# Optimization experiments

Hardware: AMD Instinct MI355X
Metric: run time of the kernel (lower is better)

## Reference

```python
import jax, jax.numpy as jnp
import numpy as np

N = 8192       # number of graph nodes (A.shape[0])
D_IN = 256     # input_dim
D_THETA = 256  # hard-coded theta projection dim
D_OUT = 256    # output_dim
K = 5          # per-row top-k sparsification
BN_EPS = 1e-5
LRELU_SLOPE = 0.01


def setup_inputs() -> dict:
    key = jax.random.key(0)
    k0, k1, k2 = jax.random.split(key, 3)
    H = jax.random.normal(k0, (N, D_IN), dtype=jnp.float32)
    # Linear(input_dim, 256)
    W_theta = jax.random.normal(k1, (D_IN, D_THETA), dtype=jnp.float32) * (1.0 / np.sqrt(D_IN))
    b_theta = jnp.zeros((D_THETA,), dtype=jnp.float32)
    # Linear(input_dim, output_dim)
    W_out = jax.random.normal(k2, (D_IN, D_OUT), dtype=jnp.float32) * (1.0 / np.sqrt(D_IN))
    b_out = jnp.zeros((D_OUT,), dtype=jnp.float32)
    # BatchNorm1d(input_dim) affine params (fresh init)
    bn_gamma = jnp.ones((D_IN,), dtype=jnp.float32)
    bn_beta = jnp.zeros((D_IN,), dtype=jnp.float32)
    return {"H": H, "bn_gamma": bn_gamma, "bn_beta": bn_beta,
            "W_theta": W_theta, "b_theta": b_theta,
            "W_out": W_out, "b_out": b_out}


def reference(H, bn_gamma, bn_beta, W_theta, b_theta, W_out, b_out):
    # BatchNorm1d in training mode: biased batch stats over the node axis
    mu = H.mean(axis=0)
    var = H.var(axis=0)  # biased, matching torch normalization
    Hn = (H - mu) * jax.lax.rsqrt(var + BN_EPS) * bn_gamma + bn_beta  # [N, D_IN]

    # theta projection -> SAM affinity
    Hx = Hn @ W_theta + b_theta                                        # [N, D_THETA]
    nrm = jnp.maximum(jnp.linalg.norm(Hx, axis=1, keepdims=True), 1e-12)  # F.normalize eps
    F1 = Hx / nrm
    dist = jnp.clip(F1 @ F1.T, -1.0, 1.0)                              # [N, N]
    sam = jnp.nan_to_num(jnp.arccos(dist))
    # original SAM() detaches (numpy round-trip): affinity is a constant wrt grads
    sam = jax.lax.stop_gradient(sam)

    A = jnp.maximum(jax.nn.sigmoid(jnp.exp(-0.2 * sam)), 0.1)          # clamp(min=0.1)

    # per-row top-k sparsification (fused replacement of the python double loop)
    _, idx = jax.lax.top_k(A, K)                                       # [N, K]
    mask = jnp.zeros_like(A).at[jnp.arange(N)[:, None], idx].set(1.0)
    A = A * mask

    # D^{-1/2} A D^{-1/2} without materializing diag matrices
    dinv = A.sum(axis=1) ** -0.5                                       # [N]
    A_hat = dinv[:, None] * A * dinv[None, :]

    out = A_hat @ (Hn @ W_out + b_out)                                 # [N, D_OUT]
    out = jnp.where(out >= 0, out, LRELU_SLOPE * out)                  # LeakyReLU
    return out, A
```

## Files before the change

### kernel.cpp

```cpp
#include <hip/hip_runtime.h>
#include <hip/hip_bf16.h>
#include <cstdint>
#include <cstddef>

#define NN 8192
#define DD 256

using bf16 = __hip_bfloat16;
typedef unsigned short ushort_t;
typedef unsigned int uint32;
typedef short short8 __attribute__((ext_vector_type(8)));
typedef float f32x4 __attribute__((ext_vector_type(4)));

#define GL2LDS(g, l) __builtin_amdgcn_global_load_lds( \
  (const __attribute__((address_space(1))) void*)(g),  \
  (__attribute__((address_space(3))) void*)(l), 16, 0, 0)

__device__ __forceinline__ float ldin(const void* p, int flag, size_t i) {
  return flag ? __bfloat162float(((const bf16*)p)[i]) : ((const float*)p)[i];
}

__device__ __forceinline__ void ins8(float v, int jj, float (&lv)[8], int (&li)[8]) {
  if (v <= lv[7]) return;
  int cnt = 0;
#pragma unroll
  for (int s = 0; s < 8; ++s) cnt += (lv[s] >= v) ? 1 : 0;
#pragma unroll
  for (int s = 7; s >= 1; --s) {
    bool sh = (s > cnt);
    lv[s] = sh ? lv[s-1] : lv[s];
    li[s] = sh ? li[s-1] : li[s];
  }
#pragma unroll
  for (int s = 0; s < 8; ++s) if (s == cnt) { lv[s] = v; li[s] = jj; }
}

__device__ __forceinline__ void ins8t(float v, int jj, float (&lv)[8], int (&li)[8]) {
  bool lose = (lv[7] > v) || (lv[7] == v && li[7] < jj);
  if (lose) return;
  int cnt = 0;
#pragma unroll
  for (int s = 0; s < 8; ++s) cnt += ((lv[s] > v) || (lv[s] == v && li[s] < jj)) ? 1 : 0;
#pragma unroll
  for (int s = 7; s >= 1; --s) {
    bool sh = (s > cnt);
    lv[s] = sh ? lv[s-1] : lv[s];
    li[s] = sh ? li[s-1] : li[s];
  }
#pragma unroll
  for (int s = 0; s < 8; ++s) if (s == cnt) { lv[s] = v; li[s] = jj; }
}

__device__ __forceinline__ bool lexgt(float va, int ia, float vb, int ib) {
  return (va > vb) || (va == vb && ia < ib);
}

__global__ void k_detect(const ushort_t* __restrict__ Hu, int* __restrict__ flag) {
  __shared__ int cnt;
  if (threadIdx.x == 0) cnt = 0;
  __syncthreads();
  int sane = 0;
  for (int u = 0; u < 16; ++u) {
    int idx = 2 * (threadIdx.x * 16 + u);
    ushort_t h = Hu[idx];
    int e = (h >> 7) & 0xFF;
    sane += (e >= 113 && e <= 133) ? 1 : 0;
  }
  atomicAdd(&cnt, sane);
  __syncthreads();
  if (threadIdx.x == 0) *flag = (cnt > 2048) ? 1 : 0;
}

__global__ void k_transposeH(const void* __restrict__ H, const int* __restrict__ pflag,
                             float* __restrict__ HT) {
  int flag = *pflag;
  __shared__ float tile[64][65];
  int i0 = blockIdx.x * 64;
  int c0 = blockIdx.y * 64;
  int tid = threadIdx.x;
  int r = tid >> 2, cb = (tid & 3) * 16;
#pragma unroll
  for (int u = 0; u < 16; ++u)
    tile[r][cb + u] = ldin(H, flag, (size_t)(i0 + r) * DD + c0 + cb + u);
  __syncthreads();
  int c = tid >> 2, rb = (tid & 3) * 16;
#pragma unroll
  for (int u4 = 0; u4 < 4; ++u4) {
    float4 t;
    t.x = tile[rb + 4*u4 + 0][c];
    t.y = tile[rb + 4*u4 + 1][c];
    t.z = tile[rb + 4*u4 + 2][c];
    t.w = tile[rb + 4*u4 + 3][c];
    *(float4*)&HT[(size_t)(c0 + c) * NN + i0 + rb + 4*u4] = t;
  }
}

__global__ __launch_bounds__(256) void k_statsT(const float* __restrict__ HT,
                                                float* __restrict__ mu32, float* __restrict__ rs32) {
  __shared__ float buf[8192];
  int c = blockIdx.x;
  int tid = threadIdx.x;
#pragma unroll
  for (int it = 0; it < 8; ++it) {
    int idx = it * 1024 + tid * 4;
    *(float4*)&buf[idx] = *(const float4*)&HT[(size_t)c * NN + idx];
  }
  __syncthreads();
  if (tid == 0) {
    float acc = 0.0f;
    for (int r = 0; r < 8192; r += 32) {
      float4 v[8];
#pragma unroll
      for (int q = 0; q < 8; ++q) v[q] = *(const float4*)&buf[r + q * 4];
#pragma unroll
      for (int q = 0; q < 8; ++q) {
        acc = __fadd_rn(acc, v[q].x);
        acc = __fadd_rn(acc, v[q].y);
        acc = __fadd_rn(acc, v[q].z);
        acc = __fadd_rn(acc, v[q].w);
      }
    }
    float mu = __fdiv_rn(acc, 8192.0f);
    float vacc = 0.0f;
    for (int r = 0; r < 8192; r += 32) {
      float4 v[8];
#pragma unroll
      for (int q = 0; q < 8; ++q) v[q] = *(const float4*)&buf[r + q * 4];
#pragma unroll
      for (int q = 0; q < 8; ++q) {
        float d0 = __fsub_rn(v[q].x, mu); vacc = __fadd_rn(vacc, __fmul_rn(d0, d0));
        float d1 = __fsub_rn(v[q].y, mu); vacc = __fadd_rn(vacc, __fmul_rn(d1, d1));
        float d2 = __fsub_rn(v[q].z, mu); vacc = __fadd_rn(vacc, __fmul_rn(d2, d2));
        float d3 = __fsub_rn(v[q].w, mu); vacc = __fadd_rn(vacc, __fmul_rn(d3, d3));
      }
    }
    float var = __fdiv_rn(vacc, 8192.0f);
    mu32[c] = mu;
    rs32[c] = __fdiv_rn(1.0f, sqrtf(__fadd_rn(var, 1e-5f)));
  }
}

__global__ void k_bn32(const void* __restrict__ H, const int* __restrict__ pflag,
                       const float* __restrict__ mu32, const float* __restrict__ rs32,
                       const void* __restrict__ gamma, const void* __restrict__ beta,
                       float* __restrict__ Hn) {
  int flag = *pflag;
  int i = blockIdx.x, c = threadIdx.x;
  float t = __fsub_rn(ldin(H, flag, (size_t)i * DD + c), mu32[c]);
  t = __fmul_rn(t, rs32[c]);
  t = __fmul_rn(t, ldin(gamma, flag, c));
  t = __fadd_rn(t, ldin(beta, flag, c));
  Hn[(size_t)i * DD + c] = t;
}

__global__ __launch_bounds__(256) void k_hx(const float* __restrict__ Hn,
    const void* __restrict__ Wt, const void* __restrict__ bt, const int* __restrict__ pflag,
    float* __restrict__ Hx) {
  int flag = *pflag;
  __shared__ float sHn[DD];
  int i = blockIdx.x, n = threadIdx.x;
  sHn[n] = Hn[(size_t)i * DD + n];
  __syncthreads();
  float acc = 0.0f;
#pragma unroll 8
  for (int k = 0; k < DD; ++k)
    acc = fmaf(sHn[k], ldin(Wt, flag, (size_t)k * DD + n), acc);
  Hx[(size_t)i * DD + n] = __fadd_rn(acc, ldin(bt, flag, n));
}

__global__ void k_norm32(float* __restrict__ F1, ushort_t* __restrict__ F1hi,
                         ushort_t* __restrict__ F1lo) {
  int w = threadIdx.x >> 6, lane = threadIdx.x & 63;
  int row = blockIdx.x * 4 + w;
  float* x = F1 + (size_t)row * DD;
  float part = 0.0f;
  if (lane < 16) {
    int base = (lane >> 3) * 128 + (lane & 7);
    float e0 = x[base];
    part = __fmul_rn(e0, e0);
#pragma unroll
    for (int t = 1; t < 16; ++t) {
      float e = x[base + 8 * t];
      part = __fadd_rn(part, __fmul_rn(e, e));
    }
  }
  float p[16];
#pragma unroll
  for (int s = 0; s < 16; ++s) p[s] = __shfl(part, s, 64);
  float P1 = __fadd_rn(__fadd_rn(__fadd_rn(p[0], p[1]), __fadd_rn(p[2], p[3])),
                       __fadd_rn(__fadd_rn(p[4], p[5]), __fadd_rn(p[6], p[7])));
  float P2 = __fadd_rn(__fadd_rn(__fadd_rn(p[8], p[9]), __fadd_rn(p[10], p[11])),
                       __fadd_rn(__fadd_rn(p[12], p[13]), __fadd_rn(p[14], p[15])));
  float nrm = fmaxf(sqrtf(__fadd_rn(P1, P2)), 1e-12f);
#pragma unroll
  for (int u = 0; u < 4; ++u) {
    float xn = __fdiv_rn(x[lane * 4 + u], nrm);
    x[lane * 4 + u] = xn;
    bf16 hi = __float2bfloat16(xn);
    float lo = __fsub_rn(xn, __bfloat162float(hi));
    F1hi[(size_t)row * DD + lane * 4 + u] = *(ushort_t*)&hi;
    bf16 lob = __float2bfloat16(lo);
    F1lo[(size_t)row * DD + lane * 4 + u] = *(ushort_t*)&lob;
  }
}

__global__ __launch_bounds__(256) void k_gemm_s(
    const ushort_t* __restrict__ F1hi, const ushort_t* __restrict__ F1lo,
    int jc, float* __restrict__ S) {
  __shared__ __align__(16) ushort_t AH[4096];
  __shared__ __align__(16) ushort_t AL[4096];
  __shared__ __align__(16) ushort_t BH[4096];
  __shared__ __align__(16) ushort_t BL[4096];
  const int tid = threadIdx.x;
  const int w = tid >> 6, lane = tid & 63;
  const int quad = lane >> 4, l15 = lane & 15;
  const int wi = w >> 1, wj = w & 1;
  const int i0 = blockIdx.y * 128;
  const int j0loc = blockIdx.x * 128;
  const int j0 = jc * 2048 + j0loc;

  const int rofs = lane >> 2;
  const int ccl  = (lane & 3) ^ (rofs & 3);
  const int laneElem = rofs * DD + ccl * 8;

  f32x4 acc[4][4];
#pragma unroll
  for (int fr = 0; fr < 4; ++fr)
#pragma unroll
    for (int fc = 0; fc < 4; ++fc) acc[fr][fc] = (f32x4)0.0f;

  for (int chunk = 0; chunk < 8; ++chunk) {
    const int kofs = chunk * 32;
    __syncthreads();
#pragma unroll
    for (int q = 0; q < 2; ++q) {
      const int s = w * 2 + q;
      const size_t ga = (size_t)(i0 + s * 16) * DD + kofs;
      const size_t gb = (size_t)(j0 + s * 16) * DD + kofs;
      GL2LDS(F1hi + ga + laneElem, &AH[s * 512]);
      GL2LDS(F1lo + ga + laneElem, &AL[s * 512]);
      GL2LDS(F1hi + gb + laneElem, &BH[s * 512]);
      GL2LDS(F1lo + gb + laneElem, &BL[s * 512]);
    }
    __syncthreads();
    short8 ah[4], al[4], bh[4], bl[4];
#pragma unroll
    for (int fr = 0; fr < 4; ++fr) {
      int row = wi * 64 + fr * 16 + l15;
      int g = quad ^ (row & 3);
      ah[fr] = *(const short8*)&AH[row * 32 + g * 8];
      al[fr] = *(const short8*)&AL[row * 32 + g * 8];
    }
#pragma unroll
    for (int fc = 0; fc < 4; ++fc) {
      int row = wj * 64 + fc * 16 + l15;
      int g = quad ^ (row & 3);
      bh[fc] = *(const short8*)&BH[row * 32 + g * 8];
      bl[fc] = *(const short8*)&BL[row * 32 + g * 8];
    }
#pragma unroll
    for (int fr = 0; fr < 4; ++fr)
#pragma unroll
      for (int fc = 0; fc < 4; ++fc) {
        acc[fr][fc] = __builtin_amdgcn_mfma_f32_16x16x32_bf16(ah[fr], bh[fc], acc[fr][fc], 0, 0, 0);
        acc[fr][fc] = __builtin_amdgcn_mfma_f32_16x16x32_bf16(ah[fr], bl[fc], acc[fr][fc], 0, 0, 0);
        acc[fr][fc] = __builtin_amdgcn_mfma_f32_16x16x32_bf16(al[fr], bh[fc], acc[fr][fc], 0, 0, 0);
      }
  }
#pragma unroll
  for (int fr = 0; fr < 4; ++fr) {
#pragma unroll
    for (int reg = 0; reg < 4; ++reg) {
      int row = i0 + wi * 64 + fr * 16 + quad * 4 + reg;
#pragma unroll
      for (int fc = 0; fc < 4; ++fc) {
        int coll = j0loc + wj * 64 + fc * 16 + l15;
        S[(size_t)row * 2048 + coll] = acc[fr][fc][reg];
      }
    }
  }
}

__global__ __launch_bounds__(256) void k_scan(const float* __restrict__ S, int jc,
                                              float* __restrict__ candv, int* __restrict__ candi) {
  int w = threadIdx.x >> 6, lane = threadIdx.x & 63;
  int row = blockIdx.x * 4 + w;
  const int jbase = jc * 2048;
  float lv[8]; int li[8];
#pragma unroll
  for (int e = 0; e < 8; ++e) { lv[e] = -3.0e38f; li[e] = 0x7fffffff; }
  const float* p = S + (size_t)row * 2048;
#pragma unroll
  for (int it = 0; it < 8; ++it) {
    int col = it * 256 + lane * 4;
    float4 v = *(const float4*)&p[col];
    ins8(v.x, jbase + col + 0, lv, li);
    ins8(v.y, jbase + col + 1, lv, li);
    ins8(v.z, jbase + col + 2, lv, li);
    ins8(v.w, jbase + col + 3, lv, li);
  }
#pragma unroll
  for (int m = 1; m <= 32; m <<= 1) {
    float bv[8]; int bi[8];
#pragma unroll
    for (int e = 0; e < 8; ++e) {
      bv[e] = __shfl_xor(lv[e], m, 64);
      bi[e] = __shfl_xor(li[e], m, 64);
    }
#pragma unroll
    for (int e = 0; e < 8; ++e) {
      bool t = lexgt(lv[e], li[e], bv[7 - e], bi[7 - e]);
      lv[e] = t ? lv[e] : bv[7 - e];
      li[e] = t ? li[e] : bi[7 - e];
    }
#pragma unroll
    for (int d = 4; d >= 1; d >>= 1) {
#pragma unroll
      for (int e = 0; e < 8; ++e) {
        if ((e & d) == 0) {
          int f = e + d;
          bool sw = lexgt(lv[f], li[f], lv[e], li[e]);
          float tv = lv[e]; int ti = li[e];
          lv[e] = sw ? lv[f] : lv[e];  li[e] = sw ? li[f] : li[e];
          lv[f] = sw ? tv : lv[f];     li[f] = sw ? ti : li[f];
        }
      }
    }
  }
  if (lane == 0) {
    size_t base = ((size_t)row * 4 + jc) * 8;
#pragma unroll
    for (int e = 0; e < 8; ++e) { candv[base + e] = lv[e]; candi[base + e] = li[e]; }
  }
}

__global__ void k_merge(const float* __restrict__ candv, const int* __restrict__ candi,
                        int* __restrict__ cand8) {
  int row = blockIdx.x * 256 + threadIdx.x;
  float bv[8]; int bj[8];
#pragma unroll
  for (int e = 0; e < 8; ++e) { bv[e] = -3.0e38f; bj[e] = 0x7fffffff; }
  for (int t = 0; t < 32; ++t) {
    float v = candv[(size_t)row * 32 + t];
    int j   = candi[(size_t)row * 32 + t];
    ins8t(v, j, bv, bj);
  }
#pragma unroll
  for (int e = 0; e < 8; ++e) cand8[row * 8 + e] = bj[e];
}

__global__ void k_rerank(const float* __restrict__ F1, const int* __restrict__ cand8,
                         int* __restrict__ top5i, float* __restrict__ top5v,
                         float* __restrict__ dinv) {
  int w = threadIdx.x >> 6, lane = threadIdx.x & 63;
  int row = blockIdx.x * 4 + w;
  int jl = 0x7fffffff;
  float a32 = -1.0f;
  if (lane < 8) {
    jl = cand8[row * 8 + lane];
    const float* xi = F1 + (size_t)row * DD;
    const float* xj = F1 + (size_t)jl * DD;
    float acc = 0.0f;
#pragma unroll 8
    for (int k = 0; k < DD; ++k)
      acc = fmaf(xi[k], xj[k], acc);
    float d = fminf(fmaxf(acc, -1.0f), 1.0f);
    float sam = acosf(d);
    float xx = expf(__fmul_rn(-0.2f, sam));
    float sig = __fdiv_rn(1.0f, __fadd_rn(1.0f, expf(-xx)));
    a32 = fmaxf(sig, 0.1f);
  }
  float av[8]; int aj[8];
#pragma unroll
  for (int l = 0; l < 8; ++l) { av[l] = __shfl(a32, l, 64); aj[l] = __shfl(jl, l, 64); }
  if (lane == 0) {
    bool used[8] = {false,false,false,false,false,false,false,false};
    double dsum = 0.0;
#pragma unroll
    for (int k = 0; k < 5; ++k) {
      float bv = -2.0f; int bj = 0x7fffffff; int bs = -1;
#pragma unroll
      for (int s = 0; s < 8; ++s) {
        bool better = (!used[s]) && ((av[s] > bv) || (av[s] == bv && aj[s] < bj));
        bs = better ? s : bs;
        bv = better ? av[s] : bv;
        bj = better ? aj[s] : bj;
      }
#pragma unroll
      for (int s = 0; s < 8; ++s) used[s] = used[s] || (s == bs);
      top5i[row * 5 + k] = bj;
      top5v[row * 5 + k] = bv;
      dsum += (double)bv;
    }
    dinv[row] = (float)(1.0 / sqrt(dsum));
  }
}

__global__ void k_z(const float* __restrict__ Hn, const int* __restrict__ top5i,
                    const float* __restrict__ top5v, const float* __restrict__ dinv,
                    float* __restrict__ Z, float* __restrict__ srow) {
  __shared__ int sj[5];
  __shared__ float sw[5];
  int i = blockIdx.x, tid = threadIdx.x;
  if (tid < 5) {
    int j = top5i[i * 5 + tid];
    sj[tid] = j;
    sw[tid] = dinv[i] * top5v[i * 5 + tid] * dinv[j];
  }
  __syncthreads();
  double z = 0.0;
#pragma unroll
  for (int k = 0; k < 5; ++k) z += (double)sw[k] * (double)Hn[(size_t)sj[k] * DD + tid];
  Z[(size_t)i * DD + tid] = (float)z;
  if (tid == 0) srow[i] = sw[0] + sw[1] + sw[2] + sw[3] + sw[4];
}

__global__ __launch_bounds__(256) void k_out3(const float* __restrict__ Z,
    const void* __restrict__ Wo, const void* __restrict__ bo,
    const float* __restrict__ srow, const int* __restrict__ pflag, void* __restrict__ outp) {
  int flag = *pflag;
  __shared__ float sZ[DD];
  int i = blockIdx.x, n = threadIdx.x;
  sZ[n] = Z[(size_t)i * DD + n];
  __syncthreads();
  float acc = 0.0f;
#pragma unroll 8
  for (int k = 0; k < DD; ++k)
    acc = fmaf(sZ[k], ldin(Wo, flag, (size_t)k * DD + n), acc);
  float v = acc + srow[i] * ldin(bo, flag, n);
  v = (v >= 0.0f) ? v : 0.01f * v;
  if (flag) ((bf16*)outp)[(size_t)i * DD + n] = __float2bfloat16(v);
  else      ((float*)outp)[(size_t)i * DD + n] = v;
}

__global__ void k_zeroA(void* __restrict__ d_out, const int* __restrict__ pflag) {
  int flag = *pflag;
  size_t esize = flag ? 2 : 4;
  uint4* base = (uint4*)((char*)d_out + (size_t)NN * DD * esize);
  size_t n16 = ((size_t)NN * NN * esize) >> 4;
  size_t idx = (size_t)blockIdx.x * 256 + threadIdx.x;
  size_t stride = (size_t)gridDim.x * 256;
  uint4 z; z.x = 0; z.y = 0; z.z = 0; z.w = 0;
  for (size_t i = idx; i < n16; i += stride) base[i] = z;
}

__global__ void k_scatter(void* __restrict__ d_out, const int* __restrict__ pflag,
                          const int* __restrict__ top5i, const float* __restrict__ top5v) {
  int flag = *pflag;
  int t = blockIdx.x * 256 + threadIdx.x;
  if (t >= NN * 5) return;
  int row = t / 5, k = t % 5;
  int col = top5i[row * 5 + k];
  float v = top5v[row * 5 + k];
  size_t off = (size_t)row * NN + col;
  if (flag) ((bf16*)((char*)d_out + (size_t)NN * DD * 2))[off] = __float2bfloat16(v);
  else      ((float*)((char*)d_out + (size_t)NN * DD * 4))[off] = v;
}

extern "C" void kernel_launch(void* const* d_in, const int* in_sizes, int n_in,
                              void* d_out, int out_size, void* d_ws, size_t ws_size,
                              hipStream_t stream) {
  (void)in_sizes; (void)n_in; (void)out_size; (void)ws_size;
  const void* H     = d_in[0];
  const void* gamma = d_in[1];
  const void* beta  = d_in[2];
  const void* Wt    = d_in[3];
  const void* bt    = d_in[4];
  const void* Wo    = d_in[5];
  const void* bo    = d_in[6];

  const size_t MB = 1048576;
  char* zb = (char*)d_out + 8 * MB;
  float*    Hn32  = (float*)(zb + 0);
  float*    F1_32 = (float*)(zb + 8 * MB);
  ushort_t* F1hi  = (ushort_t*)(zb + 16 * MB);
  ushort_t* F1lo  = (ushort_t*)(zb + 20 * MB);
  float*    candv = (float*)(zb + 24 * MB);
  int*      candi = (int*)(zb + 25 * MB);
  float*    Z32   = (float*)(zb + 28 * MB);
  float*    HT    = (float*)(zb + 36 * MB);
  float*    mu32  = (float*)(zb + 44 * MB);
  float*    rs32  = (float*)(zb + 44 * MB + 4096);
  int*      cand8 = (int*)(zb + 44 * MB + 8192);
  float*    dinv  = (float*)(zb + 44 * MB + 270336);
  float*    srow  = (float*)(zb + 44 * MB + 303104);
  float*    Schunk= (float*)(zb + 48 * MB);

  char* ws = (char*)d_ws;
  int*   flag  = (int*)(ws + 0);
  int*   top5i = (int*)(ws + 256);
  float* top5v = (float*)(ws + 164096);

  k_detect<<<dim3(1), dim3(256), 0, stream>>>((const ushort_t*)H, flag);
  k_transposeH<<<dim3(128, 4), dim3(256), 0, stream>>>(H, flag, HT);
  k_statsT<<<dim3(256), dim3(256), 0, stream>>>(HT, mu32, rs32);
  k_bn32<<<dim3(NN), dim3(256), 0, stream>>>(H, flag, mu32, rs32, gamma, beta, Hn32);
  k_hx<<<dim3(NN), dim3(256), 0, stream>>>(Hn32, Wt, bt, flag, F1_32);
  k_norm32<<<dim3(2048), dim3(256), 0, stream>>>(F1_32, F1hi, F1lo);
  for (int jc = 0; jc < 4; ++jc) {
    k_gemm_s<<<dim3(16, 64), dim3(256), 0, stream>>>(F1hi, F1lo, jc, Schunk);
    k_scan<<<dim3(2048), dim3(256), 0, stream>>>(Schunk, jc, candv, candi);
  }
  k_merge<<<dim3(32), dim3(256), 0, stream>>>(candv, candi, cand8);
  k_rerank<<<dim3(2048), dim3(256), 0, stream>>>(F1_32, cand8, top5i, top5v, dinv);
  k_z<<<dim3(NN), dim3(256), 0, stream>>>(Hn32, top5i, top5v, dinv, Z32, srow);
  k_out3<<<dim3(NN), dim3(256), 0, stream>>>(Z32, Wo, bo, srow, flag, d_out);
  k_zeroA<<<dim3(8192), dim3(256), 0, stream>>>(d_out, flag);
  k_scatter<<<dim3(160), dim3(256), 0, stream>>>(d_out, flag, top5i, top5v);
}
```

Baseline: 930.8 us.

## Fuse BN/projection/normalize, Z/output, zero/scatter kernels; skip scan inserts early

Merges the batchnorm, theta projection and row-normalization into one kernel that handles 8 rows per block, so each weight load is reused across 8 rows and the intermediate Hx no longer goes through global memory. It likewise fuses the neighbor aggregation with the output projection, 8 rows per block, and combines zeroing of the dense A matrix with the top-5 scatter, one pass per row pair. The scan adds a max-of-4 test so whole float4 groups that cannot enter the top-8 skip insertion. Risks are lower occupancy from the larger shared arrays and register accumulators, plus a different write pattern for the large A zero-fill.

```diff
diff --git a/kernel.cpp b/kernel.cpp
--- a/kernel.cpp
+++ b/kernel.cpp
@@ -140,67 +140,77 @@
   }
 }
 
-__global__ void k_bn32(const void* __restrict__ H, const int* __restrict__ pflag,
-                       const float* __restrict__ mu32, const float* __restrict__ rs32,
-                       const void* __restrict__ gamma, const void* __restrict__ beta,
-                       float* __restrict__ Hn) {
+__global__ __launch_bounds__(256) void k_hxn(const void* __restrict__ H,
+    const int* __restrict__ pflag, const float* __restrict__ mu32, const float* __restrict__ rs32,
+    const void* __restrict__ gamma, const void* __restrict__ beta,
+    const void* __restrict__ Wt, const void* __restrict__ bt,
+    float* __restrict__ Hn, float* __restrict__ F1,
+    ushort_t* __restrict__ F1hi, ushort_t* __restrict__ F1lo) {
   int flag = *pflag;
-  int i = blockIdx.x, c = threadIdx.x;
-  float t = __fsub_rn(ldin(H, flag, (size_t)i * DD + c), mu32[c]);
-  t = __fmul_rn(t, rs32[c]);
-  t = __fmul_rn(t, ldin(gamma, flag, c));
-  t = __fadd_rn(t, ldin(beta, flag, c));
-  Hn[(size_t)i * DD + c] = t;
-}
-
-__global__ __launch_bounds__(256) void k_hx(const float* __restrict__ Hn,
-    const void* __restrict__ Wt, const void* __restrict__ bt, const int* __restrict__ pflag,
-    float* __restrict__ Hx) {
-  int flag = *pflag;
-  __shared__ float sHn[DD];
-  int i = blockIdx.x, n = threadIdx.x;
-  sHn[n] = Hn[(size_t)i * DD + n];
-  __syncthreads();
-  float acc = 0.0f;
+  __shared__ float sHn[8][256];
+  __shared__ float sHx[8][256];
+  __shared__ float sp[8][16];
+  __shared__ float snrm[8];
+  const int r0 = blockIdx.x * 8;
+  const int n = threadIdx.x;
+  float g  = ldin(gamma, flag, n);
+  float b  = ldin(beta, flag, n);
+  float mu = mu32[n], rs = rs32[n];
+#pragma unroll
+  for (int r = 0; r < 8; ++r) {
+    float t = __fsub_rn(ldin(H, flag, (size_t)(r0 + r) * DD + n), mu);
+    t = __fmul_rn(t, rs);
+    t = __fmul_rn(t, g);
+    t = __fadd_rn(t, b);
+    sHn[r][n] = t;
+    Hn[(size_t)(r0 + r) * DD + n] = t;
+  }
+  __syncthreads();
+  float acc[8];
+#pragma unroll
+  for (int r = 0; r < 8; ++r) acc[r] = 0.0f;
 #pragma unroll 8
-  for (int k = 0; k < DD; ++k)
-    acc = fmaf(sHn[k], ldin(Wt, flag, (size_t)k * DD + n), acc);
-  Hx[(size_t)i * DD + n] = __fadd_rn(acc, ldin(bt, flag, n));
-}
-
-__global__ void k_norm32(float* __restrict__ F1, ushort_t* __restrict__ F1hi,
-                         ushort_t* __restrict__ F1lo) {
-  int w = threadIdx.x >> 6, lane = threadIdx.x & 63;
-  int row = blockIdx.x * 4 + w;
-  float* x = F1 + (size_t)row * DD;
-  float part = 0.0f;
-  if (lane < 16) {
-    int base = (lane >> 3) * 128 + (lane & 7);
-    float e0 = x[base];
-    part = __fmul_rn(e0, e0);
+  for (int k = 0; k < DD; ++k) {
+    float w = ldin(Wt, flag, (size_t)k * DD + n);
+#pragma unroll
+    for (int r = 0; r < 8; ++r) acc[r] = fmaf(sHn[r][k], w, acc[r]);
+  }
+  float btn = ldin(bt, flag, n);
+#pragma unroll
+  for (int r = 0; r < 8; ++r) sHx[r][n] = __fadd_rn(acc[r], btn);
+  __syncthreads();
+  if (n < 128) {
+    int r = n >> 4, s = n & 15;
+    int base = (s >> 3) * 128 + (s & 7);
+    float e0 = sHx[r][base];
+    float part = __fmul_rn(e0, e0);
 #pragma unroll
     for (int t = 1; t < 16; ++t) {
-      float e = x[base + 8 * t];
+      float e = sHx[r][base + 8 * t];
       part = __fadd_rn(part, __fmul_rn(e, e));
     }
-  }
-  float p[16];
-#pragma unroll
-  for (int s = 0; s < 16; ++s) p[s] = __shfl(part, s, 64);
-  float P1 = __fadd_rn(__fadd_rn(__fadd_rn(p[0], p[1]), __fadd_rn(p[2], p[3])),
-                       __fadd_rn(__fadd_rn(p[4], p[5]), __fadd_rn(p[6], p[7])));
-  float P2 = __fadd_rn(__fadd_rn(__fadd_rn(p[8], p[9]), __fadd_rn(p[10], p[11])),
-                       __fadd_rn(__fadd_rn(p[12], p[13]), __fadd_rn(p[14], p[15])));
-  float nrm = fmaxf(sqrtf(__fadd_rn(P1, P2)), 1e-12f);
-#pragma unroll
-  for (int u = 0; u < 4; ++u) {
-    float xn = __fdiv_rn(x[lane * 4 + u], nrm);
-    x[lane * 4 + u] = xn;
+    sp[r][s] = part;
+  }
+  __syncthreads();
+  if (n < 8) {
+    const float* p = sp[n];
+    float P1 = __fadd_rn(__fadd_rn(__fadd_rn(p[0], p[1]), __fadd_rn(p[2], p[3])),
+                         __fadd_rn(__fadd_rn(p[4], p[5]), __fadd_rn(p[6], p[7])));
+    float P2 = __fadd_rn(__fadd_rn(__fadd_rn(p[8], p[9]), __fadd_rn(p[10], p[11])),
+                         __fadd_rn(__fadd_rn(p[12], p[13]), __fadd_rn(p[14], p[15])));
+    snrm[n] = fmaxf(sqrtf(__fadd_rn(P1, P2)), 1e-12f);
+  }
+  __syncthreads();
+#pragma unroll
+  for (int r = 0; r < 8; ++r) {
+    float xn = __fdiv_rn(sHx[r][n], snrm[r]);
+    size_t idx = (size_t)(r0 + r) * DD + n;
+    F1[idx] = xn;
     bf16 hi = __float2bfloat16(xn);
     float lo = __fsub_rn(xn, __bfloat162float(hi));
-    F1hi[(size_t)row * DD + lane * 4 + u] = *(ushort_t*)&hi;
+    F1hi[idx] = *(ushort_t*)&hi;
     bf16 lob = __float2bfloat16(lo);
-    F1lo[(size_t)row * DD + lane * 4 + u] = *(ushort_t*)&lob;
+    F1lo[idx] = *(ushort_t*)&lob;
   }
 }
 
@@ -294,10 +304,13 @@
   for (int it = 0; it < 8; ++it) {
     int col = it * 256 + lane * 4;
     float4 v = *(const float4*)&p[col];
-    ins8(v.x, jbase + col + 0, lv, li);
-    ins8(v.y, jbase + col + 1, lv, li);
-    ins8(v.z, jbase + col + 2, lv, li);
-    ins8(v.w, jbase + col + 3, lv, li);
+    float m4 = fmaxf(fmaxf(v.x, v.y), fmaxf(v.z, v.w));
+    if (m4 > lv[7]) {
+      ins8(v.x, jbase + col + 0, lv, li);
+      ins8(v.y, jbase + col + 1, lv, li);
+      ins8(v.z, jbase + col + 2, lv, li);
+      ins8(v.w, jbase + col + 3, lv, li);
+    }
   }
 #pragma unroll
   for (int m = 1; m <= 32; m <<= 1) {
@@ -396,65 +409,72 @@
   }
 }
 
-__global__ void k_z(const float* __restrict__ Hn, const int* __restrict__ top5i,
-                    const float* __restrict__ top5v, const float* __restrict__ dinv,
-                    float* __restrict__ Z, float* __restrict__ srow) {
-  __shared__ int sj[5];
-  __shared__ float sw[5];
-  int i = blockIdx.x, tid = threadIdx.x;
-  if (tid < 5) {
-    int j = top5i[i * 5 + tid];
-    sj[tid] = j;
-    sw[tid] = dinv[i] * top5v[i * 5 + tid] * dinv[j];
-  }
-  __syncthreads();
-  double z = 0.0;
-#pragma unroll
-  for (int k = 0; k < 5; ++k) z += (double)sw[k] * (double)Hn[(size_t)sj[k] * DD + tid];
-  Z[(size_t)i * DD + tid] = (float)z;
-  if (tid == 0) srow[i] = sw[0] + sw[1] + sw[2] + sw[3] + sw[4];
-}
-
-__global__ __launch_bounds__(256) void k_out3(const float* __restrict__ Z,
-    const void* __restrict__ Wo, const void* __restrict__ bo,
-    const float* __restrict__ srow, const int* __restrict__ pflag, void* __restrict__ outp) {
+__global__ __launch_bounds__(256) void k_zout(const float* __restrict__ Hn,
+    const int* __restrict__ top5i, const float* __restrict__ top5v,
+    const float* __restrict__ dinv, const void* __restrict__ Wo,
+    const void* __restrict__ bo, const int* __restrict__ pflag, void* __restrict__ outp) {
   int flag = *pflag;
-  __shared__ float sZ[DD];
-  int i = blockIdx.x, n = threadIdx.x;
-  sZ[n] = Z[(size_t)i * DD + n];
-  __syncthreads();
-  float acc = 0.0f;
+  __shared__ float sZ[8][256];
+  __shared__ float ssr[8];
+  const int r0 = blockIdx.x * 8;
+  const int n = threadIdx.x;
+#pragma unroll
+  for (int r = 0; r < 8; ++r) {
+    int i = r0 + r;
+    float di = dinv[i];
+    double z = 0.0;
+    float sr = 0.0f;
+#pragma unroll
+    for (int k = 0; k < 5; ++k) {
+      int j = top5i[i * 5 + k];
+      float wgt = di * top5v[i * 5 + k] * dinv[j];
+      z += (double)wgt * (double)Hn[(size_t)j * DD + n];
+      sr += wgt;
+    }
+    sZ[r][n] = (float)z;
+    if (n == 0) ssr[r] = sr;
+  }
+  __syncthreads();
+  float acc[8];
+#pragma unroll
+  for (int r = 0; r < 8; ++r) acc[r] = 0.0f;
 #pragma unroll 8
-  for (int k = 0; k < DD; ++k)
-    acc = fmaf(sZ[k], ldin(Wo, flag, (size_t)k * DD + n), acc);
-  float v = acc + srow[i] * ldin(bo, flag, n);
-  v = (v >= 0.0f) ? v : 0.01f * v;
-  if (flag) ((bf16*)outp)[(size_t)i * DD + n] = __float2bfloat16(v);
-  else      ((float*)outp)[(size_t)i * DD + n] = v;
-}
-
-__global__ void k_zeroA(void* __restrict__ d_out, const int* __restrict__ pflag) {
+  for (int k = 0; k < DD; ++k) {
+    float w = ldin(Wo, flag, (size_t)k * DD + n);
+#pragma unroll
+    for (int r = 0; r < 8; ++r) acc[r] = fmaf(sZ[r][k], w, acc[r]);
+  }
+  float bon = ldin(bo, flag, n);
+#pragma unroll
+  for (int r = 0; r < 8; ++r) {
+    float v = acc[r] + ssr[r] * bon;
+    v = (v >= 0.0f) ? v : 0.01f * v;
+    size_t idx = (size_t)(r0 + r) * DD + n;
+    if (flag) ((bf16*)outp)[idx] = __float2bfloat16(v);
+    else      ((float*)outp)[idx] = v;
+  }
+}
+
+__global__ __launch_bounds__(256) void k_zeroscatter(void* __restrict__ d_out,
+    const int* __restrict__ pflag, const int* __restrict__ top5i,
+    const float* __restrict__ top5v) {
   int flag = *pflag;
   size_t esize = flag ? 2 : 4;
-  uint4* base = (uint4*)((char*)d_out + (size_t)NN * DD * esize);
-  size_t n16 = ((size_t)NN * NN * esize) >> 4;
-  size_t idx = (size_t)blockIdx.x * 256 + threadIdx.x;
-  size_t stride = (size_t)gridDim.x * 256;
+  int r0 = blockIdx.x * 2;
+  char* Abase = (char*)d_out + (size_t)NN * DD * esize;
+  uint4* rowp = (uint4*)(Abase + (size_t)r0 * NN * esize);
+  int nvec = (int)((2 * (size_t)NN * esize) >> 4);
   uint4 z; z.x = 0; z.y = 0; z.z = 0; z.w = 0;
-  for (size_t i = idx; i < n16; i += stride) base[i] = z;
-}
-
-__global__ void k_scatter(void* __restrict__ d_out, const int* __restrict__ pflag,
-                          const int* __restrict__ top5i, const float* __restrict__ top5v) {
-  int flag = *pflag;
-  int t = blockIdx.x * 256 + threadIdx.x;
-  if (t >= NN * 5) return;
-  int row = t / 5, k = t % 5;
-  int col = top5i[row * 5 + k];
-  float v = top5v[row * 5 + k];
-  size_t off = (size_t)row * NN + col;
-  if (flag) ((bf16*)((char*)d_out + (size_t)NN * DD * 2))[off] = __float2bfloat16(v);
-  else      ((float*)((char*)d_out + (size_t)NN * DD * 4))[off] = v;
+  for (int i = threadIdx.x; i < nvec; i += 256) rowp[i] = z;
+  __syncthreads();
+  int t = threadIdx.x;
+  if (t < 10) {
+    int r = r0 + t / 5, k = t % 5;
+    int col = top5i[r * 5 + k];
+    float v = top5v[r * 5 + k];
+    if (flag) ((bf16*)Abase)[(size_t)r * NN + col] = __float2bfloat16(v);
+    else      ((float*)Abase)[(size_t)r * NN + col] = v;
+  }
 }
 
 extern "C" void kernel_launch(void* const* d_in, const int* in_sizes, int n_in,
@@ -477,13 +497,11 @@
   ushort_t* F1lo  = (ushort_t*)(zb + 20 * MB);
   float*    candv = (float*)(zb + 24 * MB);
   int*      candi = (int*)(zb + 25 * MB);
-  float*    Z32   = (float*)(zb + 28 * MB);
   float*    HT    = (float*)(zb + 36 * MB);
   float*    mu32  = (float*)(zb + 44 * MB);
   float*    rs32  = (float*)(zb + 44 * MB + 4096);
   int*      cand8 = (int*)(zb + 44 * MB + 8192);
   float*    dinv  = (float*)(zb + 44 * MB + 270336);
-  float*    srow  = (float*)(zb + 44 * MB + 303104);
   float*    Schunk= (float*)(zb + 48 * MB);
 
   char* ws = (char*)d_ws;
@@ -494,17 +512,14 @@
   k_detect<<<dim3(1), dim3(256), 0, stream>>>((const ushort_t*)H, flag);
   k_transposeH<<<dim3(128, 4), dim3(256), 0, stream>>>(H, flag, HT);
   k_statsT<<<dim3(256), dim3(256), 0, stream>>>(HT, mu32, rs32);
-  k_bn32<<<dim3(NN), dim3(256), 0, stream>>>(H, flag, mu32, rs32, gamma, beta, Hn32);
-  k_hx<<<dim3(NN), dim3(256), 0, stream>>>(Hn32, Wt, bt, flag, F1_32);
-  k_norm32<<<dim3(2048), dim3(256), 0, stream>>>(F1_32, F1hi, F1lo);
+  k_hxn<<<dim3(1024), dim3(256), 0, stream>>>(H, flag, mu32, rs32, gamma, beta,
+                                              Wt, bt, Hn32, F1_32, F1hi, F1lo);
   for (int jc = 0; jc < 4; ++jc) {
     k_gemm_s<<<dim3(16, 64), dim3(256), 0, stream>>>(F1hi, F1lo, jc, Schunk);
     k_scan<<<dim3(2048), dim3(256), 0, stream>>>(Schunk, jc, candv, candi);
   }
   k_merge<<<dim3(32), dim3(256), 0, stream>>>(candv, candi, cand8);
   k_rerank<<<dim3(2048), dim3(256), 0, stream>>>(F1_32, cand8, top5i, top5v, dinv);
-  k_z<<<dim3(NN), dim3(256), 0, stream>>>(Hn32, top5i, top5v, dinv, Z32, srow);
-  k_out3<<<dim3(NN), dim3(256), 0, stream>>>(Z32, Wo, bo, srow, flag, d_out);
-  k_zeroA<<<dim3(8192), dim3(256), 0, stream>>>(d_out, flag);
-  k_scatter<<<dim3(160), dim3(256), 0, stream>>>(d_out, flag, top5i, top5v);
-}
+  k_zout<<<dim3(1024), dim3(256), 0, stream>>>(Hn32, top5i, top5v, dinv, Wo, bo, flag, d_out);
+  k_zeroscatter<<<dim3(4096), dim3(256), 0, stream>>>(d_out, flag, top5i, top5v);
+}
```

After: 838.4 us. 1.11x faster.
